# Kernel tuning notes

Hardware: AMD Instinct MI355X
Metric: run time of the kernel (lower is better)

## Reference

```python
import jax, jax.numpy as jnp
import numpy as np

V = 50000      # num variables (= num pos literals = num neg literals)
L = 2 * V      # num literals
C = 210000     # num clauses
E = 315000     # edges per polarity
H = 128        # hidden size
R = 4          # message-passing rounds


def _unif(k, shape, s):
    return jax.random.uniform(k, shape, jnp.float32, -s, s)


def setup_inputs() -> dict:
    key = jax.random.key(0)
    ks = jax.random.split(key, 40)
    d = {}
    d["l_embedding"] = jax.random.normal(ks[0], (L, H), jnp.float32)
    d["c_embedding"] = jax.random.normal(ks[1], (C, H), jnp.float32)
    d["edge_pos_src"] = jax.random.randint(ks[2], (E,), 0, V)
    d["edge_pos_dst"] = jax.random.randint(ks[3], (E,), 0, C)
    d["edge_neg_src"] = jax.random.randint(ks[4], (E,), 0, V)
    d["edge_neg_dst"] = jax.random.randint(ks[5], (E,), 0, C)
    s = 1.0 / np.sqrt(H)
    i = 6
    # 3-layer MLPs (Linear->ReLU->Linear->ReLU->Linear), weights stored [in, out]
    for pre in ("lmlp", "cmlp"):
        for j in range(3):
            d[f"{pre}_w{j}"] = _unif(ks[i], (H, H), s); i += 1
            d[f"{pre}_b{j}"] = _unif(ks[i], (H,), s); i += 1
    # LSTM cells: gate order i,f,g,o packed along last dim (4H)
    d["l_w_ih"] = _unif(ks[i], (2 * H, 4 * H), s); i += 1
    d["l_w_hh"] = _unif(ks[i], (H, 4 * H), s); i += 1
    d["l_b"] = _unif(ks[i], (4 * H,), s); i += 1   # b_ih + b_hh fused
    d["c_w_ih"] = _unif(ks[i], (H, 4 * H), s); i += 1
    d["c_w_hh"] = _unif(ks[i], (H, 4 * H), s); i += 1
    d["c_b"] = _unif(ks[i], (4 * H,), s); i += 1
    return d


def _mlp3(x, w0, b0, w1, b1, w2, b2):
    x = jax.nn.relu(x @ w0 + b0)
    x = jax.nn.relu(x @ w1 + b1)
    return x @ w2 + b2


def _lstm_cell(x, h, c, w_ih, w_hh, b):
    g = x @ w_ih + h @ w_hh + b          # [N, 4H]
    gi, gf, gg, go = jnp.split(g, 4, axis=-1)
    c_new = jax.nn.sigmoid(gf) * c + jax.nn.sigmoid(gi) * jnp.tanh(gg)
    h_new = jax.nn.sigmoid(go) * jnp.tanh(c_new)
    return h_new, c_new


def reference(l_embedding, c_embedding, edge_pos_src, edge_pos_dst,
              edge_neg_src, edge_neg_dst,
              lmlp_w0, lmlp_b0, lmlp_w1, lmlp_b1, lmlp_w2, lmlp_b2,
              cmlp_w0, cmlp_b0, cmlp_w1, cmlp_b1, cmlp_w2, cmlp_b2,
              l_w_ih, l_w_hh, l_b, c_w_ih, c_w_hh, c_b):
    seg = jax.ops.segment_sum
    l_h, l_c = l_embedding, jnp.zeros_like(l_embedding)
    c_h, c_c = c_embedding, jnp.zeros_like(c_embedding)
    for _ in range(R):
        # literal -> clause messages
        l_msg = _mlp3(l_h, lmlp_w0, lmlp_b0, lmlp_w1, lmlp_b1, lmlp_w2, lmlp_b2)
        pos_msg, neg_msg = jnp.split(l_msg, 2, axis=0)  # [V,H] each
        l2c = (seg(pos_msg[edge_pos_src], edge_pos_dst, num_segments=C)
               + seg(neg_msg[edge_neg_src], edge_neg_dst, num_segments=C))
        # clause -> literal messages
        c_msg = _mlp3(c_h, cmlp_w0, cmlp_b0, cmlp_w1, cmlp_b1, cmlp_w2, cmlp_b2)
        pos_c2l = seg(c_msg[edge_pos_dst], edge_pos_src, num_segments=V)
        neg_c2l = seg(c_msg[edge_neg_dst], edge_neg_src, num_segments=V)
        c2l = jnp.concatenate([pos_c2l, neg_c2l], axis=0)  # [2V,H]
        # flip literal hidden (pos <-> neg halves)
        flip = jnp.concatenate([l_h[V:], l_h[:V]], axis=0)
        # LSTM updates (seq_len=1 torch LSTM == one cell step)
        c_h, c_c = _lstm_cell(l2c, c_h, c_c, c_w_ih, c_w_hh, c_b)
        l_h, l_c = _lstm_cell(jnp.concatenate([c2l, flip], axis=1),
                              l_h, l_c, l_w_ih, l_w_hh, l_b)
    return (l_h, c_h)
```

## Files before the change

### kernel.cpp

```cpp
#include <hip/hip_runtime.h>
#include <hip/hip_bf16.h>

#define HDIM 128

using u16 = unsigned short;
using u32 = unsigned int;
using bf16x8 = __attribute__((ext_vector_type(8))) short;
using f32x4  = __attribute__((ext_vector_type(4))) float;

__device__ __forceinline__ float bf2f(u32 b) {
  union { u32 i; float f; } x; x.i = b << 16; return x.f;
}
__device__ __forceinline__ u16 f2bf(float f) {
  union { float f; u32 i; } x; x.f = f; u32 u = x.i;
  return (u16)((u + 0x7fffu + ((u >> 16) & 1u)) >> 16);
}
__device__ __forceinline__ void unpack8(uint4 r, float* o) {
  o[0] = bf2f(r.x & 0xffffu); o[1] = bf2f(r.x >> 16);
  o[2] = bf2f(r.y & 0xffffu); o[3] = bf2f(r.y >> 16);
  o[4] = bf2f(r.z & 0xffffu); o[5] = bf2f(r.z >> 16);
  o[6] = bf2f(r.w & 0xffffu); o[7] = bf2f(r.w >> 16);
}
__device__ __forceinline__ float sigm_f(float x) {
  return __builtin_amdgcn_rcpf(1.f + __expf(-x));
}
__device__ __forceinline__ float tanh_f(float x) {
  return 2.f * __builtin_amdgcn_rcpf(1.f + __expf(-2.f * x)) - 1.f;
}

__global__ __launch_bounds__(256) void k_detect(const u32* __restrict__ probe,
                                                int* __restrict__ flag) {
  __shared__ int cnt;
  if (threadIdx.x == 0) cnt = 0;
  __syncthreads();
  int local = 0;
  for (int i = threadIdx.x; i < 1024; i += 256) {
    u32 e = (probe[i] >> 7) & 0xFF;
    if (e >= 96 && e <= 126) local++;
  }
  atomicAdd(&cnt, local);
  __syncthreads();
  if (threadIdx.x == 0) *flag = (cnt > 512) ? 1 : 0;
}

__global__ __launch_bounds__(256) void k_any_to_f32(
    const void* __restrict__ src, float* __restrict__ dst, int n8,
    const int* __restrict__ flag) {
  int i = blockIdx.x * 256 + threadIdx.x;
  if (i >= n8) return;
  float t[8];
  if (*flag) {
    uint4 raw = ((const uint4*)src)[i];
    unpack8(raw, t);
  } else {
    const float4* s = ((const float4*)src) + 2 * (size_t)i;
    float4 a = s[0], b = s[1];
    t[0] = a.x; t[1] = a.y; t[2] = a.z; t[3] = a.w;
    t[4] = b.x; t[5] = b.y; t[6] = b.z; t[7] = b.w;
  }
  float4* o = ((float4*)dst) + 2 * (size_t)i;
  o[0] = make_float4(t[0], t[1], t[2], t[3]);
  o[1] = make_float4(t[4], t[5], t[6], t[7]);
}

__global__ __launch_bounds__(256) void k_any_to_bf16(
    const void* __restrict__ src, u16* __restrict__ dst, int n8,
    const int* __restrict__ flag) {
  int i = blockIdx.x * 256 + threadIdx.x;
  if (i >= n8) return;
  uint4 o;
  if (*flag) {
    o = ((const uint4*)src)[i];
  } else {
    const float4* s = ((const float4*)src) + 2 * (size_t)i;
    float4 a = s[0], b = s[1];
    o.x = (u32)f2bf(a.x) | ((u32)f2bf(a.y) << 16);
    o.y = (u32)f2bf(a.z) | ((u32)f2bf(a.w) << 16);
    o.z = (u32)f2bf(b.x) | ((u32)f2bf(b.y) << 16);
    o.w = (u32)f2bf(b.z) | ((u32)f2bf(b.w) << 16);
  }
  ((uint4*)dst)[i] = o;
}

__global__ __launch_bounds__(256) void k_build_wt(
    const void* __restrict__ Wih, const void* __restrict__ Whh, int KX, int Ktot,
    int Ncols, u16* __restrict__ WT, const int* __restrict__ flag) {
  int idx = blockIdx.x * 256 + threadIdx.x;
  int total = Ncols * Ktot;
  if (idx >= total) return;
  int n = idx / Ktot, k = idx - n * Ktot;
  const void* src = (k < KX) ? Wih : Whh;
  int kk = (k < KX) ? k : k - KX;
  size_t off = (size_t)kk * Ncols + n;
  u16 b;
  if (*flag) b = ((const u16*)src)[off];
  else       b = f2bf(((const float*)src)[off]);
  WT[(size_t)n * Ktot + k] = b;
}

__global__ __launch_bounds__(256) void k_sentinel(float* __restrict__ out,
                                                  int n, float val) {
  int i = blockIdx.x * 256 + threadIdx.x;
  if (i < n) out[i] = val;
}

__global__ __launch_bounds__(256) void k_count(
    const int* __restrict__ key, int key_add, int E, int* __restrict__ deg) {
  int e = blockIdx.x * 256 + threadIdx.x;
  if (e < E) atomicAdd(&deg[key[e] + key_add], 1);
}

__global__ __launch_bounds__(256) void k_scan1(
    const int* __restrict__ in, int* __restrict__ inc,
    int* __restrict__ bsum, int n) {
  __shared__ int s[256];
  const int tid = threadIdx.x;
  const int b0 = blockIdx.x * 1024;
  int v[4]; int sum = 0;
#pragma unroll
  for (int j = 0; j < 4; ++j) {
    int i = b0 + tid * 4 + j;
    int x = (i < n) ? in[i] : 0;
    sum += x; v[j] = sum;
  }
  s[tid] = sum;
  __syncthreads();
  for (int d = 1; d < 256; d <<= 1) {
    int t = (tid >= d) ? s[tid - d] : 0;
    __syncthreads();
    s[tid] += t;
    __syncthreads();
  }
  int base = (tid > 0) ? s[tid - 1] : 0;
#pragma unroll
  for (int j = 0; j < 4; ++j) {
    int i = b0 + tid * 4 + j;
    if (i < n) inc[i] = base + v[j];
  }
  if (tid == 255) bsum[blockIdx.x] = s[255];
}

__global__ __launch_bounds__(256) void k_scan2(int* __restrict__ bsum, int nb) {
  __shared__ int s[256];
  const int tid = threadIdx.x;
  int x = (tid < nb) ? bsum[tid] : 0;
  s[tid] = x;
  __syncthreads();
  for (int d = 1; d < 256; d <<= 1) {
    int t = (tid >= d) ? s[tid - d] : 0;
    __syncthreads();
    s[tid] += t;
    __syncthreads();
  }
  if (tid < nb) bsum[tid] = (tid > 0) ? s[tid - 1] : 0;
}

__global__ __launch_bounds__(256) void k_scan3(
    const int* __restrict__ inc, const int* __restrict__ bsum,
    int* __restrict__ off, int* __restrict__ cursor, int n) {
  int i = blockIdx.x * 256 + threadIdx.x;
  if (i < n) {
    int v = inc[i] + bsum[i >> 10];
    off[i + 1] = v;
    int prev = (i & 1023) ? (inc[i - 1] + bsum[i >> 10]) : bsum[i >> 10];
    cursor[i] = prev;
    if (i == 0) { off[0] = 0; cursor[0] = 0; }
  }
}

__global__ __launch_bounds__(256) void k_fill(
    const int* __restrict__ key, int key_add,
    const int* __restrict__ pay, int pay_add, int E,
    int* __restrict__ cursor, int* __restrict__ vals) {
  int e = blockIdx.x * 256 + threadIdx.x;
  if (e >= E) return;
  int k = key[e] + key_add;
  int p = atomicAdd(&cursor[k], 1);
  vals[p] = pay[e] + pay_add;
}

__global__ __launch_bounds__(256) void k_mlp3(
    const u16* __restrict__ X, u16* __restrict__ Y, int N,
    const u16* __restrict__ WT0, const float* __restrict__ B0,
    const u16* __restrict__ WT1, const float* __restrict__ B1,
    const u16* __restrict__ WT2, const float* __restrict__ B2) {
  __shared__ u16 xs[128 * 128];
  const int tid = threadIdx.x;
  const int lane = tid & 63;
  const int w = tid >> 6;
  const int lr = lane & 15;
  const int hi = lane >> 4;
  const int lk = hi * 8;
  const int row0 = blockIdx.x * 128;

  {
    const int row = tid >> 1, half = tid & 1;
    const int grow = row0 + row;
#pragma unroll
    for (int j = 0; j < 8; ++j) {
      int g = half * 8 + j;
      uint4 v = {0, 0, 0, 0};
      if (grow < N) v = *reinterpret_cast<const uint4*>(X + (size_t)grow * HDIM + g * 8);
      ((uint4*)xs)[row * 16 + (g ^ (row & 7))] = v;
    }
  }
  __syncthreads();

  const u16* WTs[3] = {WT0, WT1, WT2};
  const float* Bs[3] = {B0, B1, B2};
#pragma unroll
  for (int layer = 0; layer < 3; ++layer) {
    f32x4 zc = {0.f, 0.f, 0.f, 0.f};
    f32x4 acc[8][2];
#pragma unroll
    for (int rt = 0; rt < 8; ++rt) { acc[rt][0] = zc; acc[rt][1] = zc; }
#pragma unroll
    for (int ks = 0; ks < 4; ++ks) {
      bf16x8 bfr[2];
#pragma unroll
      for (int t = 0; t < 2; ++t) {
        int col = w * 32 + t * 16 + lr;
        bfr[t] = *reinterpret_cast<const bf16x8*>(
            WTs[layer] + (size_t)col * HDIM + ks * 32 + lk);
      }
#pragma unroll
      for (int rt = 0; rt < 8; ++rt) {
        int row = rt * 16 + lr;
        int g = ks * 4 + hi;
        bf16x8 a = ((const bf16x8*)xs)[row * 16 + (g ^ (row & 7))];
        acc[rt][0] = __builtin_amdgcn_mfma_f32_16x16x32_bf16(a, bfr[0], acc[rt][0], 0, 0, 0);
        acc[rt][1] = __builtin_amdgcn_mfma_f32_16x16x32_bf16(a, bfr[1], acc[rt][1], 0, 0, 0);
      }
    }
    float bv[2];
    bv[0] = Bs[layer][w * 32 + lr];
    bv[1] = Bs[layer][w * 32 + 16 + lr];
    __syncthreads();
    if (layer < 2) {
#pragma unroll
      for (int rt = 0; rt < 8; ++rt)
#pragma unroll
        for (int t = 0; t < 2; ++t) {
          int col = w * 32 + t * 16 + lr;
          int g = col >> 3, cw = col & 7;
#pragma unroll
          for (int reg = 0; reg < 4; ++reg) {
            int row = rt * 16 + hi * 4 + reg;
            float v = fmaxf(acc[rt][t][reg] + bv[t], 0.f);
            xs[(row * 16 + (g ^ (row & 7))) * 8 + cw] = f2bf(v);
          }
        }
      __syncthreads();
    } else {
#pragma unroll
      for (int rt = 0; rt < 8; ++rt)
#pragma unroll
        for (int t = 0; t < 2; ++t) {
          int col = w * 32 + t * 16 + lr;
#pragma unroll
          for (int reg = 0; reg < 4; ++reg) {
            int row = row0 + rt * 16 + hi * 4 + reg;
            if (row < N) Y[(size_t)row * HDIM + col] = f2bf(acc[rt][t][reg] + bv[t]);
          }
        }
    }
  }
}

template<int HAS_X1, int OUT_F32, int FIRST, int LAST>
__global__ __launch_bounds__(512) void k_lstm3(
    const u16* __restrict__ msgs, const int* __restrict__ moff,
    const int* __restrict__ mvals,
    const u16* __restrict__ X1, int Vhalf,
    const u16* __restrict__ Hin, const float* __restrict__ Cin,
    void* __restrict__ Hout, float* __restrict__ Cout,
    const u16* __restrict__ WT, const float* __restrict__ Bias, int N) {
  const int KT = HAS_X1 ? 384 : 256;
  const int KS = KT / 32;
  const int G = KT / 8;
  __shared__ u16 xs[64 * (HAS_X1 ? 384 : 256)];
  const int tid = threadIdx.x;
  const int lane = tid & 63;
  const int w = tid >> 6;
  const int lr = lane & 15;
  const int hi = lane >> 4;
  const int lk = hi * 8;
  const int row0 = blockIdx.x * 64;

  {
    const int row = tid >> 3, sub = tid & 7;
    const int grow = row0 + row;
    const int swz = row & 7;
    uint4* lds = (uint4*)xs + row * G;
    int s0 = 0, s1 = 0;
    if (grow < N) { s0 = moff[grow]; s1 = moff[grow + 1]; }
    uint4 vh = {0, 0, 0, 0}, vx = {0, 0, 0, 0};
    if (grow < N) {
      vh = *reinterpret_cast<const uint4*>(Hin + (size_t)grow * HDIM + sub * 16);
    }
    uint4 vh1 = {0, 0, 0, 0}, vx1 = {0, 0, 0, 0};
    if (grow < N) {
      vh1 = *reinterpret_cast<const uint4*>(Hin + (size_t)grow * HDIM + sub * 16 + 8);
      if (HAS_X1) {
        int sr = (grow < Vhalf) ? grow + Vhalf : grow - Vhalf;
        vx  = *reinterpret_cast<const uint4*>(X1 + (size_t)sr * HDIM + sub * 16);
        vx1 = *reinterpret_cast<const uint4*>(X1 + (size_t)sr * HDIM + sub * 16 + 8);
      }
    }
    float a[16];
#pragma unroll
    for (int t = 0; t < 16; ++t) a[t] = 0.f;
    {
      int j = s0;
      for (; j + 1 < s1; j += 2) {
        int v0 = mvals[j], v1 = mvals[j + 1];
        const uint4* p0 = reinterpret_cast<const uint4*>(msgs + (size_t)v0 * HDIM + sub * 16);
        const uint4* p1 = reinterpret_cast<const uint4*>(msgs + (size_t)v1 * HDIM + sub * 16);
        uint4 r0 = p0[0], r1 = p0[1], r2 = p1[0], r3 = p1[1];
        float f0[8], f1[8], f2[8], f3[8];
        unpack8(r0, f0); unpack8(r1, f1); unpack8(r2, f2); unpack8(r3, f3);
#pragma unroll
        for (int t = 0; t < 8; ++t) {
          a[t]     += f0[t] + f2[t];
          a[8 + t] += f1[t] + f3[t];
        }
      }
      if (j < s1) {
        const uint4* p = reinterpret_cast<const uint4*>(msgs + (size_t)mvals[j] * HDIM + sub * 16);
        uint4 r0 = p[0], r1 = p[1];
        float f0[8], f1[8];
        unpack8(r0, f0); unpack8(r1, f1);
#pragma unroll
        for (int t = 0; t < 8; ++t) { a[t] += f0[t]; a[8 + t] += f1[t]; }
      }
    }
    uint4 pk;
    pk.x = (u32)f2bf(a[0]) | ((u32)f2bf(a[1]) << 16);
    pk.y = (u32)f2bf(a[2]) | ((u32)f2bf(a[3]) << 16);
    pk.z = (u32)f2bf(a[4]) | ((u32)f2bf(a[5]) << 16);
    pk.w = (u32)f2bf(a[6]) | ((u32)f2bf(a[7]) << 16);
    lds[(sub * 2) ^ swz] = pk;
    pk.x = (u32)f2bf(a[8])  | ((u32)f2bf(a[9])  << 16);
    pk.y = (u32)f2bf(a[10]) | ((u32)f2bf(a[11]) << 16);
    pk.z = (u32)f2bf(a[12]) | ((u32)f2bf(a[13]) << 16);
    pk.w = (u32)f2bf(a[14]) | ((u32)f2bf(a[15]) << 16);
    lds[(sub * 2 + 1) ^ swz] = pk;
    if (HAS_X1) {
      lds[(16 + sub * 2) ^ swz] = vx;
      lds[(16 + sub * 2 + 1) ^ swz] = vx1;
    }
    {
      int gb = (HAS_X1 ? 32 : 16) + sub * 2;
      lds[gb ^ swz] = vh;
      lds[(gb + 1) ^ swz] = vh1;
    }
  }
  __syncthreads();

  f32x4 zc = {0.f, 0.f, 0.f, 0.f};
  f32x4 acc[4][4];
#pragma unroll
  for (int rt = 0; rt < 4; ++rt)
#pragma unroll
    for (int q = 0; q < 4; ++q) acc[rt][q] = zc;

#pragma unroll
  for (int ks = 0; ks < KS; ++ks) {
    bf16x8 bfr[4];
#pragma unroll
    for (int q = 0; q < 4; ++q) {
      int col = q * 128 + w * 16 + lr;
      bfr[q] = *reinterpret_cast<const bf16x8*>(WT + (size_t)col * KT + ks * 32 + lk);
    }
#pragma unroll
    for (int rt = 0; rt < 4; ++rt) {
      int row = rt * 16 + lr;
      bf16x8 a = ((const bf16x8*)xs)[row * G + ((ks * 4 + hi) ^ (row & 7))];
#pragma unroll
      for (int q = 0; q < 4; ++q)
        acc[rt][q] = __builtin_amdgcn_mfma_f32_16x16x32_bf16(a, bfr[q], acc[rt][q], 0, 0, 0);
    }
  }

  const int m = w * 16 + lr;
  float bv[4];
#pragma unroll
  for (int q = 0; q < 4; ++q) bv[q] = Bias[q * 128 + m];

  if (row0 + 64 <= N) {
#pragma unroll
    for (int rt = 0; rt < 4; ++rt) {
      size_t cb = ((size_t)((row0 >> 4) + rt) * 128 + m) * 16 + hi * 4;
      float4 cin = make_float4(0.f, 0.f, 0.f, 0.f);
      if (!FIRST) cin = *reinterpret_cast<const float4*>(Cin + cb);
      float4 cout;
      float hn[4];
#pragma unroll
      for (int reg = 0; reg < 4; ++reg) {
        float gi = acc[rt][0][reg] + bv[0];
        float gf = acc[rt][1][reg] + bv[1];
        float gg = acc[rt][2][reg] + bv[2];
        float go = acc[rt][3][reg] + bv[3];
        float co = (&cin.x)[reg];
        float cn = sigm_f(gf) * co + sigm_f(gi) * tanh_f(gg);
        hn[reg] = sigm_f(go) * tanh_f(cn);
        (&cout.x)[reg] = cn;
      }
      if (!LAST) *reinterpret_cast<float4*>(Cout + cb) = cout;
      int rowb = row0 + rt * 16 + hi * 4;
#pragma unroll
      for (int reg = 0; reg < 4; ++reg) {
        size_t hidx = (size_t)(rowb + reg) * HDIM + m;
        if (OUT_F32) ((float*)Hout)[hidx] = hn[reg];
        else         ((u16*)Hout)[hidx]   = f2bf(hn[reg]);
      }
    }
  } else {
#pragma unroll
    for (int rt = 0; rt < 4; ++rt)
#pragma unroll
      for (int reg = 0; reg < 4; ++reg) {
        int row = row0 + rt * 16 + hi * 4 + reg;
        if (row >= N) continue;
        size_t cb = ((size_t)(row >> 4) * 128 + m) * 16 + (row & 15);
        float gi = acc[rt][0][reg] + bv[0];
        float gf = acc[rt][1][reg] + bv[1];
        float gg = acc[rt][2][reg] + bv[2];
        float go = acc[rt][3][reg] + bv[3];
        float co = FIRST ? 0.f : Cin[cb];
        float cn = sigm_f(gf) * co + sigm_f(gi) * tanh_f(gg);
        float hn = sigm_f(go) * tanh_f(cn);
        if (!LAST) Cout[cb] = cn;
        size_t hidx = (size_t)row * HDIM + m;
        if (OUT_F32) ((float*)Hout)[hidx] = hn;
        else         ((u16*)Hout)[hidx]   = f2bf(hn);
      }
  }
}

extern "C" void kernel_launch(void* const* d_in, const int* in_sizes, int n_in,
                              void* d_out, int out_size, void* d_ws, size_t ws_size,
                              hipStream_t stream) {
  const int V = in_sizes[0] / (2 * HDIM);
  const int L = 2 * V;
  const int C = in_sizes[1] / HDIM;
  const int E = in_sizes[2];
  const int R = 4;

  const void* l_emb = d_in[0];
  const void* c_emb = d_in[1];
  const int* eps  = (const int*)d_in[2];
  const int* epd  = (const int*)d_in[3];
  const int* ens  = (const int*)d_in[4];
  const int* end_ = (const int*)d_in[5];

  const size_t LH = (size_t)L * HDIM;
  const size_t CH = (size_t)C * HDIM;

  char* base = (char*)d_ws;
  auto alloc = [&](size_t bytes) -> char* {
    char* r = base; base += (bytes + 255) / 256 * 256; return r;
  };
  u16* l_hA  = (u16*)alloc(LH * 2);
  u16* l_hB  = (u16*)alloc(LH * 2);
  u16* c_h   = (u16*)alloc(CH * 2);
  u16* tL    = (u16*)alloc(LH * 2);
  u16* tC    = (u16*)alloc(CH * 2);
  float* l_c = (float*)alloc(LH * 4);
  float* c_c = (float*)alloc(CH * 4);
  u16* WT_lmlp[3]; u16* WT_cmlp[3];
  for (int j = 0; j < 3; ++j) WT_lmlp[j] = (u16*)alloc(HDIM * HDIM * 2);
  for (int j = 0; j < 3; ++j) WT_cmlp[j] = (u16*)alloc(HDIM * HDIM * 2);
  u16* WT_l = (u16*)alloc(512 * 384 * 2);
  u16* WT_c = (u16*)alloc(512 * 256 * 2);
  float* Bf_lmlp[3]; float* Bf_cmlp[3];
  for (int j = 0; j < 3; ++j) Bf_lmlp[j] = (float*)alloc(HDIM * 4);
  for (int j = 0; j < 3; ++j) Bf_cmlp[j] = (float*)alloc(HDIM * 4);
  float* Bf_l = (float*)alloc(512 * 4);
  float* Bf_c = (float*)alloc(512 * 4);
  int* deg1 = (int*)alloc((size_t)C * 4);
  int* off1 = (int*)alloc(((size_t)C + 1) * 4);
  int* cur1 = (int*)alloc((size_t)C * 4);
  int* vals1 = (int*)alloc((size_t)2 * E * 4);
  int* deg2 = (int*)alloc((size_t)L * 4);
  int* off2 = (int*)alloc(((size_t)L + 1) * 4);
  int* cur2 = (int*)alloc((size_t)L * 4);
  int* vals2 = (int*)alloc((size_t)2 * E * 4);
  int* inc  = (int*)alloc((size_t)(C > L ? C : L) * 4);
  int* bsum = (int*)alloc(256 * 4);
  int* flag = (int*)alloc(256);

  size_t required = (size_t)(base - (char*)d_ws);
  if (required > ws_size) {
    float val = 64.0f + (float)(ws_size >> 26);
    k_sentinel<<<(out_size + 255) / 256, 256, 0, stream>>>((float*)d_out, out_size, val);
    return;
  }

  k_detect<<<1, 256, 0, stream>>>((const u32*)d_in[6], flag);
  const int mlp_tot = HDIM * HDIM;
  for (int j = 0; j < 3; ++j) {
    k_build_wt<<<(mlp_tot + 255) / 256, 256, 0, stream>>>(
        d_in[6 + 2 * j], d_in[6 + 2 * j], HDIM, HDIM, HDIM, WT_lmlp[j], flag);
    k_build_wt<<<(mlp_tot + 255) / 256, 256, 0, stream>>>(
        d_in[12 + 2 * j], d_in[12 + 2 * j], HDIM, HDIM, HDIM, WT_cmlp[j], flag);
  }
  k_build_wt<<<(512 * 384 + 255) / 256, 256, 0, stream>>>(
      d_in[18], d_in[19], 256, 384, 512, WT_l, flag);
  k_build_wt<<<(512 * 256 + 255) / 256, 256, 0, stream>>>(
      d_in[21], d_in[22], 128, 256, 512, WT_c, flag);
  k_any_to_f32<<<1, 256, 0, stream>>>(d_in[7],  Bf_lmlp[0], HDIM / 8, flag);
  k_any_to_f32<<<1, 256, 0, stream>>>(d_in[9],  Bf_lmlp[1], HDIM / 8, flag);
  k_any_to_f32<<<1, 256, 0, stream>>>(d_in[11], Bf_lmlp[2], HDIM / 8, flag);
  k_any_to_f32<<<1, 256, 0, stream>>>(d_in[13], Bf_cmlp[0], HDIM / 8, flag);
  k_any_to_f32<<<1, 256, 0, stream>>>(d_in[15], Bf_cmlp[1], HDIM / 8, flag);
  k_any_to_f32<<<1, 256, 0, stream>>>(d_in[17], Bf_cmlp[2], HDIM / 8, flag);
  k_any_to_f32<<<1, 256, 0, stream>>>(d_in[20], Bf_l, 512 / 8, flag);
  k_any_to_f32<<<1, 256, 0, stream>>>(d_in[23], Bf_c, 512 / 8, flag);

  const int gE = (E + 255) / 256;
  (void)hipMemsetAsync(deg1, 0, (size_t)C * 4, stream);
  (void)hipMemsetAsync(deg2, 0, (size_t)L * 4, stream);
  k_count<<<gE, 256, 0, stream>>>(epd, 0, E, deg1);
  k_count<<<gE, 256, 0, stream>>>(end_, 0, E, deg1);
  k_count<<<gE, 256, 0, stream>>>(eps, 0, E, deg2);
  k_count<<<gE, 256, 0, stream>>>(ens, V, E, deg2);
  {
    int nb = (C + 1023) / 1024;
    k_scan1<<<nb, 256, 0, stream>>>(deg1, inc, bsum, C);
    k_scan2<<<1, 256, 0, stream>>>(bsum, nb);
    k_scan3<<<(C + 255) / 256, 256, 0, stream>>>(inc, bsum, off1, cur1, C);
  }
  {
    int nb = (L + 1023) / 1024;
    k_scan1<<<nb, 256, 0, stream>>>(deg2, inc, bsum, L);
    k_scan2<<<1, 256, 0, stream>>>(bsum, nb);
    k_scan3<<<(L + 255) / 256, 256, 0, stream>>>(inc, bsum, off2, cur2, L);
  }
  k_fill<<<gE, 256, 0, stream>>>(epd, 0, eps, 0, E, cur1, vals1);
  k_fill<<<gE, 256, 0, stream>>>(end_, 0, ens, V, E, cur1, vals1);
  k_fill<<<gE, 256, 0, stream>>>(eps, 0, epd, 0, E, cur2, vals2);
  k_fill<<<gE, 256, 0, stream>>>(ens, V, end_, 0, E, cur2, vals2);

  k_any_to_bf16<<<(int)((LH / 8 + 255) / 256), 256, 0, stream>>>(l_emb, l_hA, (int)(LH / 8), flag);
  k_any_to_bf16<<<(int)((CH / 8 + 255) / 256), 256, 0, stream>>>(c_emb, c_h, (int)(CH / 8), flag);

  u16* lh_cur = l_hA;
  u16* lh_nxt = l_hB;
  float* outf = (float*)d_out;

  const int gm_l = (L + 127) / 128;
  const int gm_c = (C + 127) / 128;
  const int gs_c = (C + 63) / 64;
  const int gs_l = (L + 63) / 64;

  for (int r = 0; r < R; ++r) {
    k_mlp3<<<gm_l, 256, 0, stream>>>(lh_cur, tL, L,
        WT_lmlp[0], Bf_lmlp[0], WT_lmlp[1], Bf_lmlp[1], WT_lmlp[2], Bf_lmlp[2]);
    k_mlp3<<<gm_c, 256, 0, stream>>>(c_h, tC, C,
        WT_cmlp[0], Bf_cmlp[0], WT_cmlp[1], Bf_cmlp[1], WT_cmlp[2], Bf_cmlp[2]);
    if (r == 0) {
      k_lstm3<0, 0, 1, 0><<<gs_c, 512, 0, stream>>>(
          tL, off1, vals1, (const u16*)nullptr, 0, c_h, c_c,
          (void*)c_h, c_c, WT_c, Bf_c, C);
      k_lstm3<1, 0, 1, 0><<<gs_l, 512, 0, stream>>>(
          tC, off2, vals2, lh_cur, V, lh_cur, l_c,
          (void*)lh_nxt, l_c, WT_l, Bf_l, L);
      u16* tmp = lh_cur; lh_cur = lh_nxt; lh_nxt = tmp;
    } else if (r == R - 1) {
      k_lstm3<0, 1, 0, 1><<<gs_c, 512, 0, stream>>>(
          tL, off1, vals1, (const u16*)nullptr, 0, c_h, c_c,
          (void*)(outf + LH), c_c, WT_c, Bf_c, C);
      k_lstm3<1, 1, 0, 1><<<gs_l, 512, 0, stream>>>(
          tC, off2, vals2, lh_cur, V, lh_cur, l_c,
          (void*)outf, l_c, WT_l, Bf_l, L);
    } else {
      k_lstm3<0, 0, 0, 0><<<gs_c, 512, 0, stream>>>(
          tL, off1, vals1, (const u16*)nullptr, 0, c_h, c_c,
          (void*)c_h, c_c, WT_c, Bf_c, C);
      k_lstm3<1, 0, 0, 0><<<gs_l, 512, 0, stream>>>(
          tC, off2, vals2, lh_cur, V, lh_cur, l_c,
          (void*)lh_nxt, l_c, WT_l, Bf_l, L);
      u16* tmp = lh_cur; lh_cur = lh_nxt; lh_nxt = tmp;
    }
  }
}
```

Measured before the change: 1.876 ms.

## Store LSTM cell state in bf16 and shrink MLP tile to 64 rows

```diff
diff --git a/kernel.cpp b/kernel.cpp
--- a/kernel.cpp
+++ b/kernel.cpp
@@ -179,26 +179,26 @@
   vals[p] = pay[e] + pay_add;
 }
 
-__global__ __launch_bounds__(256) void k_mlp3(
+__global__ __launch_bounds__(256, 8) void k_mlp3(
     const u16* __restrict__ X, u16* __restrict__ Y, int N,
     const u16* __restrict__ WT0, const float* __restrict__ B0,
     const u16* __restrict__ WT1, const float* __restrict__ B1,
     const u16* __restrict__ WT2, const float* __restrict__ B2) {
-  __shared__ u16 xs[128 * 128];
+  __shared__ u16 xs[64 * 128];
   const int tid = threadIdx.x;
   const int lane = tid & 63;
   const int w = tid >> 6;
   const int lr = lane & 15;
   const int hi = lane >> 4;
   const int lk = hi * 8;
-  const int row0 = blockIdx.x * 128;
+  const int row0 = blockIdx.x * 64;
 
   {
-    const int row = tid >> 1, half = tid & 1;
+    const int row = tid >> 2, q = tid & 3;
     const int grow = row0 + row;
 #pragma unroll
-    for (int j = 0; j < 8; ++j) {
-      int g = half * 8 + j;
+    for (int j = 0; j < 4; ++j) {
+      int g = q * 4 + j;
       uint4 v = {0, 0, 0, 0};
       if (grow < N) v = *reinterpret_cast<const uint4*>(X + (size_t)grow * HDIM + g * 8);
       ((uint4*)xs)[row * 16 + (g ^ (row & 7))] = v;
@@ -211,9 +211,9 @@
 #pragma unroll
   for (int layer = 0; layer < 3; ++layer) {
     f32x4 zc = {0.f, 0.f, 0.f, 0.f};
-    f32x4 acc[8][2];
-#pragma unroll
-    for (int rt = 0; rt < 8; ++rt) { acc[rt][0] = zc; acc[rt][1] = zc; }
+    f32x4 acc[4][2];
+#pragma unroll
+    for (int rt = 0; rt < 4; ++rt) { acc[rt][0] = zc; acc[rt][1] = zc; }
 #pragma unroll
     for (int ks = 0; ks < 4; ++ks) {
       bf16x8 bfr[2];
@@ -224,10 +224,9 @@
             WTs[layer] + (size_t)col * HDIM + ks * 32 + lk);
       }
 #pragma unroll
-      for (int rt = 0; rt < 8; ++rt) {
+      for (int rt = 0; rt < 4; ++rt) {
         int row = rt * 16 + lr;
-        int g = ks * 4 + hi;
-        bf16x8 a = ((const bf16x8*)xs)[row * 16 + (g ^ (row & 7))];
+        bf16x8 a = ((const bf16x8*)xs)[row * 16 + ((ks * 4 + hi) ^ (row & 7))];
         acc[rt][0] = __builtin_amdgcn_mfma_f32_16x16x32_bf16(a, bfr[0], acc[rt][0], 0, 0, 0);
         acc[rt][1] = __builtin_amdgcn_mfma_f32_16x16x32_bf16(a, bfr[1], acc[rt][1], 0, 0, 0);
       }
@@ -238,7 +237,7 @@
     __syncthreads();
     if (layer < 2) {
 #pragma unroll
-      for (int rt = 0; rt < 8; ++rt)
+      for (int rt = 0; rt < 4; ++rt)
 #pragma unroll
         for (int t = 0; t < 2; ++t) {
           int col = w * 32 + t * 16 + lr;
@@ -253,7 +252,7 @@
       __syncthreads();
     } else {
 #pragma unroll
-      for (int rt = 0; rt < 8; ++rt)
+      for (int rt = 0; rt < 4; ++rt)
 #pragma unroll
         for (int t = 0; t < 2; ++t) {
           int col = w * 32 + t * 16 + lr;
@@ -272,8 +271,8 @@
     const u16* __restrict__ msgs, const int* __restrict__ moff,
     const int* __restrict__ mvals,
     const u16* __restrict__ X1, int Vhalf,
-    const u16* __restrict__ Hin, const float* __restrict__ Cin,
-    void* __restrict__ Hout, float* __restrict__ Cout,
+    const u16* __restrict__ Hin, const u16* __restrict__ Cin,
+    void* __restrict__ Hout, u16* __restrict__ Cout,
     const u16* __restrict__ WT, const float* __restrict__ Bias, int N) {
   const int KT = HAS_X1 ? 384 : 256;
   const int KS = KT / 32;
@@ -295,11 +294,9 @@
     int s0 = 0, s1 = 0;
     if (grow < N) { s0 = moff[grow]; s1 = moff[grow + 1]; }
     uint4 vh = {0, 0, 0, 0}, vx = {0, 0, 0, 0};
-    if (grow < N) {
-      vh = *reinterpret_cast<const uint4*>(Hin + (size_t)grow * HDIM + sub * 16);
-    }
     uint4 vh1 = {0, 0, 0, 0}, vx1 = {0, 0, 0, 0};
     if (grow < N) {
+      vh  = *reinterpret_cast<const uint4*>(Hin + (size_t)grow * HDIM + sub * 16);
       vh1 = *reinterpret_cast<const uint4*>(Hin + (size_t)grow * HDIM + sub * 16 + 8);
       if (HAS_X1) {
         int sr = (grow < Vhalf) ? grow + Vhalf : grow - Vhalf;
@@ -391,22 +388,28 @@
 #pragma unroll
     for (int rt = 0; rt < 4; ++rt) {
       size_t cb = ((size_t)((row0 >> 4) + rt) * 128 + m) * 16 + hi * 4;
-      float4 cin = make_float4(0.f, 0.f, 0.f, 0.f);
-      if (!FIRST) cin = *reinterpret_cast<const float4*>(Cin + cb);
-      float4 cout;
-      float hn[4];
+      float cin[4] = {0.f, 0.f, 0.f, 0.f};
+      if (!FIRST) {
+        uint2 cr = *reinterpret_cast<const uint2*>(Cin + cb);
+        cin[0] = bf2f(cr.x & 0xffffu); cin[1] = bf2f(cr.x >> 16);
+        cin[2] = bf2f(cr.y & 0xffffu); cin[3] = bf2f(cr.y >> 16);
+      }
+      float cn[4], hn[4];
 #pragma unroll
       for (int reg = 0; reg < 4; ++reg) {
         float gi = acc[rt][0][reg] + bv[0];
         float gf = acc[rt][1][reg] + bv[1];
         float gg = acc[rt][2][reg] + bv[2];
         float go = acc[rt][3][reg] + bv[3];
-        float co = (&cin.x)[reg];
-        float cn = sigm_f(gf) * co + sigm_f(gi) * tanh_f(gg);
-        hn[reg] = sigm_f(go) * tanh_f(cn);
-        (&cout.x)[reg] = cn;
-      }
-      if (!LAST) *reinterpret_cast<float4*>(Cout + cb) = cout;
+        cn[reg] = sigm_f(gf) * cin[reg] + sigm_f(gi) * tanh_f(gg);
+        hn[reg] = sigm_f(go) * tanh_f(cn[reg]);
+      }
+      if (!LAST) {
+        uint2 cw;
+        cw.x = (u32)f2bf(cn[0]) | ((u32)f2bf(cn[1]) << 16);
+        cw.y = (u32)f2bf(cn[2]) | ((u32)f2bf(cn[3]) << 16);
+        *reinterpret_cast<uint2*>(Cout + cb) = cw;
+      }
       int rowb = row0 + rt * 16 + hi * 4;
 #pragma unroll
       for (int reg = 0; reg < 4; ++reg) {
@@ -427,10 +430,10 @@
         float gf = acc[rt][1][reg] + bv[1];
         float gg = acc[rt][2][reg] + bv[2];
         float go = acc[rt][3][reg] + bv[3];
-        float co = FIRST ? 0.f : Cin[cb];
+        float co = FIRST ? 0.f : bf2f((u32)Cin[cb]);
         float cn = sigm_f(gf) * co + sigm_f(gi) * tanh_f(gg);
         float hn = sigm_f(go) * tanh_f(cn);
-        if (!LAST) Cout[cb] = cn;
+        if (!LAST) Cout[cb] = f2bf(cn);
         size_t hidx = (size_t)row * HDIM + m;
         if (OUT_F32) ((float*)Hout)[hidx] = hn;
         else         ((u16*)Hout)[hidx]   = f2bf(hn);
@@ -466,8 +469,8 @@
   u16* c_h   = (u16*)alloc(CH * 2);
   u16* tL    = (u16*)alloc(LH * 2);
   u16* tC    = (u16*)alloc(CH * 2);
-  float* l_c = (float*)alloc(LH * 4);
-  float* c_c = (float*)alloc(CH * 4);
+  u16* l_c   = (u16*)alloc(LH * 2);
+  u16* c_c   = (u16*)alloc(CH * 2);
   u16* WT_lmlp[3]; u16* WT_cmlp[3];
   for (int j = 0; j < 3; ++j) WT_lmlp[j] = (u16*)alloc(HDIM * HDIM * 2);
   for (int j = 0; j < 3; ++j) WT_cmlp[j] = (u16*)alloc(HDIM * HDIM * 2);
@@ -549,8 +552,8 @@
   u16* lh_nxt = l_hB;
   float* outf = (float*)d_out;
 
-  const int gm_l = (L + 127) / 128;
-  const int gm_c = (C + 127) / 128;
+  const int gm_l = (L + 63) / 64;
+  const int gm_c = (C + 63) / 64;
   const int gs_c = (C + 63) / 64;
   const int gs_l = (L + 63) / 64;
 
```

Measured after the change: 1.970 ms. +5.0%, slower.

## Pair pos/neg literal rows per block to reuse hidden state as flip input

Applied to the files above, without the earlier changes.

```diff
diff --git a/kernel.cpp b/kernel.cpp
--- a/kernel.cpp
+++ b/kernel.cpp
@@ -267,18 +267,17 @@
   }
 }
 
-template<int HAS_X1, int OUT_F32, int FIRST, int LAST>
+template<int OUT_F32, int FIRST, int LAST>
 __global__ __launch_bounds__(512) void k_lstm3(
     const u16* __restrict__ msgs, const int* __restrict__ moff,
     const int* __restrict__ mvals,
-    const u16* __restrict__ X1, int Vhalf,
     const u16* __restrict__ Hin, const float* __restrict__ Cin,
     void* __restrict__ Hout, float* __restrict__ Cout,
     const u16* __restrict__ WT, const float* __restrict__ Bias, int N) {
-  const int KT = HAS_X1 ? 384 : 256;
+  const int KT = 256;
   const int KS = KT / 32;
   const int G = KT / 8;
-  __shared__ u16 xs[64 * (HAS_X1 ? 384 : 256)];
+  __shared__ u16 xs[64 * 256];
   const int tid = threadIdx.x;
   const int lane = tid & 63;
   const int w = tid >> 6;
@@ -294,18 +293,10 @@
     uint4* lds = (uint4*)xs + row * G;
     int s0 = 0, s1 = 0;
     if (grow < N) { s0 = moff[grow]; s1 = moff[grow + 1]; }
-    uint4 vh = {0, 0, 0, 0}, vx = {0, 0, 0, 0};
+    uint4 vh = {0, 0, 0, 0}, vh1 = {0, 0, 0, 0};
     if (grow < N) {
-      vh = *reinterpret_cast<const uint4*>(Hin + (size_t)grow * HDIM + sub * 16);
-    }
-    uint4 vh1 = {0, 0, 0, 0}, vx1 = {0, 0, 0, 0};
-    if (grow < N) {
+      vh  = *reinterpret_cast<const uint4*>(Hin + (size_t)grow * HDIM + sub * 16);
       vh1 = *reinterpret_cast<const uint4*>(Hin + (size_t)grow * HDIM + sub * 16 + 8);
-      if (HAS_X1) {
-        int sr = (grow < Vhalf) ? grow + Vhalf : grow - Vhalf;
-        vx  = *reinterpret_cast<const uint4*>(X1 + (size_t)sr * HDIM + sub * 16);
-        vx1 = *reinterpret_cast<const uint4*>(X1 + (size_t)sr * HDIM + sub * 16 + 8);
-      }
     }
     float a[16];
 #pragma unroll
@@ -345,12 +336,8 @@
     pk.z = (u32)f2bf(a[12]) | ((u32)f2bf(a[13]) << 16);
     pk.w = (u32)f2bf(a[14]) | ((u32)f2bf(a[15]) << 16);
     lds[(sub * 2 + 1) ^ swz] = pk;
-    if (HAS_X1) {
-      lds[(16 + sub * 2) ^ swz] = vx;
-      lds[(16 + sub * 2 + 1) ^ swz] = vx1;
-    }
     {
-      int gb = (HAS_X1 ? 32 : 16) + sub * 2;
+      int gb = 16 + sub * 2;
       lds[gb ^ swz] = vh;
       lds[(gb + 1) ^ swz] = vh1;
     }
@@ -438,6 +425,174 @@
   }
 }
 
+template<int OUT_F32, int FIRST, int LAST>
+__global__ __launch_bounds__(512) void k_lstm_lit(
+    const u16* __restrict__ msgs, const int* __restrict__ moff,
+    const int* __restrict__ mvals,
+    const u16* __restrict__ Hglob, const u16* __restrict__ Cin,
+    void* __restrict__ Hout, u16* __restrict__ Cout,
+    const u16* __restrict__ WT, const float* __restrict__ Bias, int V) {
+  const int KT = 384;
+  __shared__ u16 xs[64 * 256];
+  const int tid = threadIdx.x;
+  const int lane = tid & 63;
+  const int w = tid >> 6;
+  const int lr = lane & 15;
+  const int hi = lane >> 4;
+  const int lk = hi * 8;
+  const int rb = blockIdx.x * 32;
+
+  {
+    const int row = tid >> 3, sub = tid & 7;
+    const int offh = (row < 32) ? row : (row - 32);
+    const int g = (row < 32) ? (rb + row) : (V + rb + row - 32);
+    const bool valid = (rb + offh) < V;
+    const int swz = row & 7;
+    uint4* lds = (uint4*)xs + row * 32;
+    int s0 = 0, s1 = 0;
+    if (valid) { s0 = moff[g]; s1 = moff[g + 1]; }
+    uint4 vh = {0, 0, 0, 0}, vh1 = {0, 0, 0, 0};
+    if (valid) {
+      vh  = *reinterpret_cast<const uint4*>(Hglob + (size_t)g * HDIM + sub * 16);
+      vh1 = *reinterpret_cast<const uint4*>(Hglob + (size_t)g * HDIM + sub * 16 + 8);
+    }
+    float a[16];
+#pragma unroll
+    for (int t = 0; t < 16; ++t) a[t] = 0.f;
+    {
+      int j = s0;
+      for (; j + 1 < s1; j += 2) {
+        int v0 = mvals[j], v1 = mvals[j + 1];
+        const uint4* p0 = reinterpret_cast<const uint4*>(msgs + (size_t)v0 * HDIM + sub * 16);
+        const uint4* p1 = reinterpret_cast<const uint4*>(msgs + (size_t)v1 * HDIM + sub * 16);
+        uint4 r0 = p0[0], r1 = p0[1], r2 = p1[0], r3 = p1[1];
+        float f0[8], f1[8], f2[8], f3[8];
+        unpack8(r0, f0); unpack8(r1, f1); unpack8(r2, f2); unpack8(r3, f3);
+#pragma unroll
+        for (int t = 0; t < 8; ++t) {
+          a[t]     += f0[t] + f2[t];
+          a[8 + t] += f1[t] + f3[t];
+        }
+      }
+      if (j < s1) {
+        const uint4* p = reinterpret_cast<const uint4*>(msgs + (size_t)mvals[j] * HDIM + sub * 16);
+        uint4 r0 = p[0], r1 = p[1];
+        float f0[8], f1[8];
+        unpack8(r0, f0); unpack8(r1, f1);
+#pragma unroll
+        for (int t = 0; t < 8; ++t) { a[t] += f0[t]; a[8 + t] += f1[t]; }
+      }
+    }
+    uint4 pk;
+    pk.x = (u32)f2bf(a[0]) | ((u32)f2bf(a[1]) << 16);
+    pk.y = (u32)f2bf(a[2]) | ((u32)f2bf(a[3]) << 16);
+    pk.z = (u32)f2bf(a[4]) | ((u32)f2bf(a[5]) << 16);
+    pk.w = (u32)f2bf(a[6]) | ((u32)f2bf(a[7]) << 16);
+    lds[(sub * 2) ^ swz] = pk;
+    pk.x = (u32)f2bf(a[8])  | ((u32)f2bf(a[9])  << 16);
+    pk.y = (u32)f2bf(a[10]) | ((u32)f2bf(a[11]) << 16);
+    pk.z = (u32)f2bf(a[12]) | ((u32)f2bf(a[13]) << 16);
+    pk.w = (u32)f2bf(a[14]) | ((u32)f2bf(a[15]) << 16);
+    lds[(sub * 2 + 1) ^ swz] = pk;
+    lds[16 + ((sub * 2) ^ swz)] = vh;
+    lds[16 + ((sub * 2 + 1) ^ swz)] = vh1;
+  }
+  __syncthreads();
+
+  f32x4 zc = {0.f, 0.f, 0.f, 0.f};
+  f32x4 acc[4][4];
+#pragma unroll
+  for (int rt = 0; rt < 4; ++rt)
+#pragma unroll
+    for (int q = 0; q < 4; ++q) acc[rt][q] = zc;
+
+  const bf16x8* lds16 = (const bf16x8*)xs;
+#pragma unroll
+  for (int ks = 0; ks < 12; ++ks) {
+    bf16x8 bfr[4];
+#pragma unroll
+    for (int q = 0; q < 4; ++q) {
+      int col = q * 128 + w * 16 + lr;
+      bfr[q] = *reinterpret_cast<const bf16x8*>(WT + (size_t)col * KT + ks * 32 + lk);
+    }
+#pragma unroll
+    for (int rt = 0; rt < 4; ++rt) {
+      int row = rt * 16 + lr;
+      int swz = row & 7;
+      bf16x8 a;
+      if (ks < 4)       a = lds16[row * 32 + ((ks * 4 + hi) ^ swz)];
+      else if (ks < 8)  a = lds16[(row ^ 32) * 32 + 16 + (((ks - 4) * 4 + hi) ^ swz)];
+      else              a = lds16[row * 32 + 16 + (((ks - 8) * 4 + hi) ^ swz)];
+#pragma unroll
+      for (int q = 0; q < 4; ++q)
+        acc[rt][q] = __builtin_amdgcn_mfma_f32_16x16x32_bf16(a, bfr[q], acc[rt][q], 0, 0, 0);
+    }
+  }
+
+  const int m = w * 16 + lr;
+  float bv[4];
+#pragma unroll
+  for (int q = 0; q < 4; ++q) bv[q] = Bias[q * 128 + m];
+
+  if (rb + 32 <= V) {
+#pragma unroll
+    for (int rt = 0; rt < 4; ++rt) {
+      int gb = (rt < 2) ? (rb + rt * 16) : (V + rb + (rt - 2) * 16);
+      size_t cb = ((size_t)(gb >> 4) * 128 + m) * 16 + hi * 4;
+      float cin[4] = {0.f, 0.f, 0.f, 0.f};
+      if (!FIRST) {
+        uint2 cr = *reinterpret_cast<const uint2*>(Cin + cb);
+        cin[0] = bf2f(cr.x & 0xffffu); cin[1] = bf2f(cr.x >> 16);
+        cin[2] = bf2f(cr.y & 0xffffu); cin[3] = bf2f(cr.y >> 16);
+      }
+      float cn[4], hn[4];
+#pragma unroll
+      for (int reg = 0; reg < 4; ++reg) {
+        float gi = acc[rt][0][reg] + bv[0];
+        float gf = acc[rt][1][reg] + bv[1];
+        float gg = acc[rt][2][reg] + bv[2];
+        float go = acc[rt][3][reg] + bv[3];
+        cn[reg] = sigm_f(gf) * cin[reg] + sigm_f(gi) * tanh_f(gg);
+        hn[reg] = sigm_f(go) * tanh_f(cn[reg]);
+      }
+      if (!LAST) {
+        uint2 cw;
+        cw.x = (u32)f2bf(cn[0]) | ((u32)f2bf(cn[1]) << 16);
+        cw.y = (u32)f2bf(cn[2]) | ((u32)f2bf(cn[3]) << 16);
+        *reinterpret_cast<uint2*>(Cout + cb) = cw;
+      }
+#pragma unroll
+      for (int reg = 0; reg < 4; ++reg) {
+        size_t hidx = (size_t)(gb + hi * 4 + reg) * HDIM + m;
+        if (OUT_F32) ((float*)Hout)[hidx] = hn[reg];
+        else         ((u16*)Hout)[hidx]   = f2bf(hn[reg]);
+      }
+    }
+  } else {
+#pragma unroll
+    for (int rt = 0; rt < 4; ++rt)
+#pragma unroll
+      for (int reg = 0; reg < 4; ++reg) {
+        int lrow = rt * 16 + hi * 4 + reg;
+        int offh = (lrow < 32) ? lrow : (lrow - 32);
+        if (rb + offh >= V) continue;
+        int g = (lrow < 32) ? (rb + lrow) : (V + rb + lrow - 32);
+        size_t cb = ((size_t)(g >> 4) * 128 + m) * 16 + (g & 15);
+        float gi = acc[rt][0][reg] + bv[0];
+        float gf = acc[rt][1][reg] + bv[1];
+        float gg = acc[rt][2][reg] + bv[2];
+        float go = acc[rt][3][reg] + bv[3];
+        float co = FIRST ? 0.f : bf2f((u32)Cin[cb]);
+        float cn = sigm_f(gf) * co + sigm_f(gi) * tanh_f(gg);
+        float hn = sigm_f(go) * tanh_f(cn);
+        if (!LAST) Cout[cb] = f2bf(cn);
+        size_t hidx = (size_t)g * HDIM + m;
+        if (OUT_F32) ((float*)Hout)[hidx] = hn;
+        else         ((u16*)Hout)[hidx]   = f2bf(hn);
+      }
+  }
+}
+
 extern "C" void kernel_launch(void* const* d_in, const int* in_sizes, int n_in,
                               void* d_out, int out_size, void* d_ws, size_t ws_size,
                               hipStream_t stream) {
@@ -466,7 +621,7 @@
   u16* c_h   = (u16*)alloc(CH * 2);
   u16* tL    = (u16*)alloc(LH * 2);
   u16* tC    = (u16*)alloc(CH * 2);
-  float* l_c = (float*)alloc(LH * 4);
+  u16* l_c   = (u16*)alloc(LH * 2);
   float* c_c = (float*)alloc(CH * 4);
   u16* WT_lmlp[3]; u16* WT_cmlp[3];
   for (int j = 0; j < 3; ++j) WT_lmlp[j] = (u16*)alloc(HDIM * HDIM * 2);
@@ -552,7 +707,7 @@
   const int gm_l = (L + 127) / 128;
   const int gm_c = (C + 127) / 128;
   const int gs_c = (C + 63) / 64;
-  const int gs_l = (L + 63) / 64;
+  const int gs_l = (V + 31) / 32;
 
   for (int r = 0; r < R; ++r) {
     k_mlp3<<<gm_l, 256, 0, stream>>>(lh_cur, tL, L,
@@ -560,27 +715,21 @@
     k_mlp3<<<gm_c, 256, 0, stream>>>(c_h, tC, C,
         WT_cmlp[0], Bf_cmlp[0], WT_cmlp[1], Bf_cmlp[1], WT_cmlp[2], Bf_cmlp[2]);
     if (r == 0) {
-      k_lstm3<0, 0, 1, 0><<<gs_c, 512, 0, stream>>>(
-          tL, off1, vals1, (const u16*)nullptr, 0, c_h, c_c,
-          (void*)c_h, c_c, WT_c, Bf_c, C);
-      k_lstm3<1, 0, 1, 0><<<gs_l, 512, 0, stream>>>(
-          tC, off2, vals2, lh_cur, V, lh_cur, l_c,
-          (void*)lh_nxt, l_c, WT_l, Bf_l, L);
+      k_lstm3<0, 1, 0><<<gs_c, 512, 0, stream>>>(
+          tL, off1, vals1, c_h, c_c, (void*)c_h, c_c, WT_c, Bf_c, C);
+      k_lstm_lit<0, 1, 0><<<gs_l, 512, 0, stream>>>(
+          tC, off2, vals2, lh_cur, l_c, (void*)lh_nxt, l_c, WT_l, Bf_l, V);
       u16* tmp = lh_cur; lh_cur = lh_nxt; lh_nxt = tmp;
     } else if (r == R - 1) {
-      k_lstm3<0, 1, 0, 1><<<gs_c, 512, 0, stream>>>(
-          tL, off1, vals1, (const u16*)nullptr, 0, c_h, c_c,
-          (void*)(outf + LH), c_c, WT_c, Bf_c, C);
-      k_lstm3<1, 1, 0, 1><<<gs_l, 512, 0, stream>>>(
-          tC, off2, vals2, lh_cur, V, lh_cur, l_c,
-          (void*)outf, l_c, WT_l, Bf_l, L);
+      k_lstm3<1, 0, 1><<<gs_c, 512, 0, stream>>>(
+          tL, off1, vals1, c_h, c_c, (void*)(outf + LH), c_c, WT_c, Bf_c, C);
+      k_lstm_lit<1, 0, 1><<<gs_l, 512, 0, stream>>>(
+          tC, off2, vals2, lh_cur, l_c, (void*)outf, l_c, WT_l, Bf_l, V);
     } else {
-      k_lstm3<0, 0, 0, 0><<<gs_c, 512, 0, stream>>>(
-          tL, off1, vals1, (const u16*)nullptr, 0, c_h, c_c,
-          (void*)c_h, c_c, WT_c, Bf_c, C);
-      k_lstm3<1, 0, 0, 0><<<gs_l, 512, 0, stream>>>(
-          tC, off2, vals2, lh_cur, V, lh_cur, l_c,
-          (void*)lh_nxt, l_c, WT_l, Bf_l, L);
+      k_lstm3<0, 0, 0><<<gs_c, 512, 0, stream>>>(
+          tL, off1, vals1, c_h, c_c, (void*)c_h, c_c, WT_c, Bf_c, C);
+      k_lstm_lit<0, 0, 0><<<gs_l, 512, 0, stream>>>(
+          tC, off2, vals2, lh_cur, l_c, (void*)lh_nxt, l_c, WT_l, Bf_l, V);
       u16* tmp = lh_cur; lh_cur = lh_nxt; lh_nxt = tmp;
     }
   }
```

New measurement: 1.943 ms. +3.6%, slower.
